# Optimization experiments

Measured on AMD Instinct MI355X. Metric: run time of the kernel, lower is better.

## Reference

```python
import jax, jax.numpy as jnp
import numpy as np

B, N, IN_DIM = 32, 8192, 128
H, C = 4, 32
NEG_SLOPE = 0.2


def _xavier(key, shape, fan_in, fan_out):
    limit = np.sqrt(6.0 / (fan_in + fan_out))
    return jax.random.uniform(key, shape, minval=-limit, maxval=limit, dtype=jnp.float32)


def setup_inputs() -> dict:
    key = jax.random.key(0)
    k_x, k_wl, k_wr, k_att = jax.random.split(key, 4)
    x = jax.random.normal(k_x, (B, N, IN_DIM), dtype=jnp.float32)
    W_l = _xavier(k_wl, (IN_DIM, H * C), IN_DIM, H * C)
    b_l = jnp.zeros((H * C,), dtype=jnp.float32)
    W_r = _xavier(k_wr, (IN_DIM, H * C), IN_DIM, H * C)
    b_r = jnp.zeros((H * C,), dtype=jnp.float32)
    att = _xavier(k_att, (H, C), H, C)
    return {"x": x, "W_l": W_l, "b_l": b_l, "W_r": W_r, "b_r": b_r, "att": att}


def reference(x, W_l, b_l, W_r, b_r, att):
    Bs, Ns, _ = x.shape
    # Dense projections -> [B, N, H, C]
    x_l = (x @ W_l + b_l).reshape(Bs, Ns, H, C)
    x_r = (x @ W_r + b_r).reshape(Bs, Ns, H, C)
    # GATv2 additive score for edges (j -> center 0): LeakyReLU(x_l[0] + x_r[j])
    e = jax.nn.leaky_relu(x_l[:, :1, :, :] + x_r, negative_slope=NEG_SLOPE)  # [B,N,H,C]
    logits = jnp.einsum('bnhc,hc->bnh', e, att)  # [B,N,H]
    alpha = jax.nn.softmax(logits, axis=1)
    # Weighted aggregation into the center node; others keep their self-loop x_r
    m_center = jnp.sum(alpha[..., None] * x_r, axis=1, keepdims=True)  # [B,1,H,C]
    out = x_r.at[:, :1, :, :].set(m_center)
    return out.reshape(Bs, Ns, H * C)
```

## Files before the change

kernel.cpp:

```cpp
#include <hip/hip_runtime.h>

#define BATCH 32
#define NROWS 8192
#define IND   128
#define HC    128
#define NEG   0.2f
#define NBLK  32
#define ROWS  64
#define ITERS (NROWS / (NBLK * ROWS))
#define PART_STRIDE 136

typedef __attribute__((ext_vector_type(8))) short short8;
typedef __attribute__((ext_vector_type(4))) float f32x4;

__device__ __forceinline__ unsigned short f2bf(float f) {
    unsigned u = __float_as_uint(f);
    u += 0x7FFFu + ((u >> 16) & 1u);
    return (unsigned short)(u >> 16);
}
__device__ __forceinline__ unsigned pack2(float a, float b) {
    return (unsigned)f2bf(a) | ((unsigned)f2bf(b) << 16);
}

__global__ void gat_center(const float* __restrict__ x, const float* __restrict__ Wl,
                           const float* __restrict__ bl, float* __restrict__ xl0)
{
    const int b = blockIdx.x, t = threadIdx.x;
    __shared__ float xrow[128];
    xrow[t] = x[(size_t)b * NROWS * IND + t];
    __syncthreads();
    float acc = bl[t];
#pragma unroll 16
    for (int k = 0; k < 128; ++k) acc = fmaf(xrow[k], Wl[k * 128 + t], acc);
    xl0[b * 128 + t] = acc;
}

__global__ __launch_bounds__(256, 2) void gat_main(
    const float* __restrict__ x, const float* __restrict__ Wr,
    const float* __restrict__ br, const float* __restrict__ att,
    const float* __restrict__ xl0, float* __restrict__ out,
    float* __restrict__ part)
{
    const int tid  = threadIdx.x;
    const int lane = tid & 63;
    const int wv   = tid >> 6;
    const int b    = blockIdx.x >> 5;
    const int blk  = blockIdx.x & (NBLK - 1);

    __shared__ unsigned short WrT[128 * 128];
    __shared__ float ubuf[64 * 132];
    __shared__ float w_s[64][4];
    __shared__ float wmax_s[4][4];
    __shared__ float wsum_s[4][4];
    __shared__ float Mrun_s[4], Srun_s[4], scale_s[4];
    __shared__ float Prun_s[128];
    __shared__ float ptmp_s[2][128];
    __shared__ float xl0_s[128], att_s[128], br_s[128];

    unsigned short* Asw = (unsigned short*)ubuf;
    float (*xr_s)[132]  = (float(*)[132])ubuf;

    for (int i = tid; i < 128 * 128; i += 256) {
        int n = i & 127, k = i >> 7;
        WrT[n * 128 + (k ^ ((n & 7) << 3))] = f2bf(Wr[k * 128 + n]);
    }
    if (tid < 128) {
        xl0_s[tid]  = xl0[b * 128 + tid];
        att_s[tid]  = att[tid];
        br_s[tid]   = br[tid];
        Prun_s[tid] = 0.f;
    }
    if (tid < 4) { Mrun_s[tid] = -INFINITY; Srun_s[tid] = 0.f; }
    __syncthreads();

    const int lr = tid >> 2, lh = tid & 3;

    for (int it = 0; it < ITERS; ++it) {
        const int n0 = blk * (ITERS * ROWS) + it * ROWS;
        const float* xrow0 = x + ((size_t)b * NROWS + n0) * IND;

#pragma unroll
        for (int ii = 0; ii < 4; ++ii) {
            int ci = tid + ii * 256;
            int r  = ci >> 4;
            int kc = (ci & 15) << 3;
            float4 f0 = *(const float4*)(xrow0 + r * IND + kc);
            float4 f1 = *(const float4*)(xrow0 + r * IND + kc + 4);
            uint4 u;
            u.x = pack2(f0.x, f0.y); u.y = pack2(f0.z, f0.w);
            u.z = pack2(f1.x, f1.y); u.w = pack2(f1.z, f1.w);
            *(uint4*)&Asw[r * 128 + (kc ^ ((r & 7) << 3))] = u;
        }
        __syncthreads();

        f32x4 acc[8];
#pragma unroll
        for (int i = 0; i < 8; ++i) acc[i] = (f32x4){0.f, 0.f, 0.f, 0.f};
        {
            const int rA   = wv * 16 + (lane & 15);
            const int ksel = lane >> 4;
            short8 afr[4];
#pragma unroll
            for (int ks = 0; ks < 4; ++ks) {
                int k0 = ks * 32 + ksel * 8;
                afr[ks] = *(const short8*)&Asw[rA * 128 + (k0 ^ ((rA & 7) << 3))];
            }
            const int nb = lane & 15;
#pragma unroll
            for (int nt = 0; nt < 8; ++nt) {
                const int n = nt * 16 + nb;
                const unsigned short* bp = &WrT[n * 128];
                const int sw = (n & 7) << 3;
#pragma unroll
                for (int ks = 0; ks < 4; ++ks) {
                    int k0 = ks * 32 + ksel * 8;
                    short8 bfr = *(const short8*)&bp[k0 ^ sw];
                    acc[nt] = __builtin_amdgcn_mfma_f32_16x16x32_bf16(afr[ks], bfr, acc[nt], 0, 0, 0);
                }
            }
        }
        __syncthreads();

        {
            const int rowb = wv * 16 + (lane >> 4) * 4;
            const int colb = lane & 15;
#pragma unroll
            for (int nt = 0; nt < 8; ++nt) {
                const int col  = nt * 16 + colb;
                const float bias = br_s[col];
#pragma unroll
                for (int rg = 0; rg < 4; ++rg)
                    xr_s[rowb + rg][col] = acc[nt][rg] + bias;
            }
        }
        __syncthreads();

        {
            float* ob = out + ((size_t)b * NROWS + n0) * HC;
#pragma unroll
            for (int j = 0; j < 8; ++j) {
                int idx = tid + j * 256;
                int row = idx >> 5, c4 = (idx & 31) << 2;
                *(float4*)(ob + row * HC + c4) = *(const float4*)&xr_s[row][c4];
            }
        }

        float lg = 0.f;
        {
            const float* xp = &xr_s[lr][lh * 32];
            const float* ap = &att_s[lh * 32];
            const float* qp = &xl0_s[lh * 32];
#pragma unroll
            for (int c4 = 0; c4 < 32; c4 += 4) {
                float4 xv = *(const float4*)(xp + c4);
                float4 av = *(const float4*)(ap + c4);
                float4 qv = *(const float4*)(qp + c4);
                float v0 = qv.x + xv.x; v0 = v0 > 0.f ? v0 : NEG * v0;
                float v1 = qv.y + xv.y; v1 = v1 > 0.f ? v1 : NEG * v1;
                float v2 = qv.z + xv.z; v2 = v2 > 0.f ? v2 : NEG * v2;
                float v3 = qv.w + xv.w; v3 = v3 > 0.f ? v3 : NEG * v3;
                lg = fmaf(v0, av.x, fmaf(v1, av.y, fmaf(v2, av.z, fmaf(v3, av.w, lg))));
            }
        }

        float mx = lg;
#pragma unroll
        for (int mk = 4; mk < 64; mk <<= 1) mx = fmaxf(mx, __shfl_xor(mx, mk));
        if (lane < 4) wmax_s[wv][lane] = mx;
        __syncthreads();

        const float Mblk = fmaxf(fmaxf(wmax_s[0][lh], wmax_s[1][lh]),
                                 fmaxf(wmax_s[2][lh], wmax_s[3][lh]));
        const float Mold = Mrun_s[lh];
        const float Mnew = fmaxf(Mold, Mblk);
        const float w    = __expf(lg - Mnew);
        w_s[lr][lh] = w;
        float swv = w;
#pragma unroll
        for (int mk = 4; mk < 64; mk <<= 1) swv += __shfl_xor(swv, mk);
        if (lane < 4) wsum_s[wv][lane] = swv;
        __syncthreads();

        if (tid < 4) {
            const float sc = __expf(Mold - Mnew);
            scale_s[tid] = sc;
            Srun_s[tid]  = Srun_s[tid] * sc +
                (wsum_s[0][tid] + wsum_s[1][tid] + wsum_s[2][tid] + wsum_s[3][tid]);
            Mrun_s[tid]  = Mnew;
        }
        {
            const int hc = tid & 127, half = tid >> 7;
            const int h2 = hc >> 5;
            float accp = 0.f;
#pragma unroll 8
            for (int i2 = 0; i2 < 32; ++i2) {
                int rr = half * 32 + i2;
                accp = fmaf(w_s[rr][h2], xr_s[rr][hc], accp);
            }
            ptmp_s[half][hc] = accp;
        }
        __syncthreads();
        if (tid < 128)
            Prun_s[tid] = Prun_s[tid] * scale_s[tid >> 5] + ptmp_s[0][tid] + ptmp_s[1][tid];
        __syncthreads();
    }

    float* pb = part + (size_t)(b * NBLK + blk) * PART_STRIDE;
    if (tid < 4)   { pb[tid] = Mrun_s[tid]; pb[4 + tid] = Srun_s[tid]; }
    if (tid < 128) pb[8 + tid] = Prun_s[tid];
}

__global__ void gat_final(const float* __restrict__ part, float* __restrict__ out)
{
    const int b = blockIdx.x, t = threadIdx.x;
    const int h = t >> 5;
    const float* pb = part + (size_t)b * NBLK * PART_STRIDE;
    float Mg = -INFINITY;
    for (int i = 0; i < NBLK; ++i) Mg = fmaxf(Mg, pb[i * PART_STRIDE + h]);
    float Sg = 0.f, Pg = 0.f;
    for (int i = 0; i < NBLK; ++i) {
        const float sc = __expf(pb[i * PART_STRIDE + h] - Mg);
        Sg += pb[i * PART_STRIDE + 4 + h] * sc;
        Pg  = fmaf(pb[i * PART_STRIDE + 8 + t], sc, Pg);
    }
    out[(size_t)b * NROWS * HC + t] = Pg / Sg;
}

extern "C" void kernel_launch(void* const* d_in, const int* in_sizes, int n_in,
                              void* d_out, int out_size, void* d_ws, size_t ws_size,
                              hipStream_t stream)
{
    const float* x   = (const float*)d_in[0];
    const float* Wl  = (const float*)d_in[1];
    const float* bl  = (const float*)d_in[2];
    const float* Wr  = (const float*)d_in[3];
    const float* br  = (const float*)d_in[4];
    const float* att = (const float*)d_in[5];
    float* out = (float*)d_out;

    float* xl0  = (float*)d_ws;
    float* part = xl0 + BATCH * 128;

    gat_center<<<BATCH, 128, 0, stream>>>(x, Wl, bl, xl0);
    gat_main<<<BATCH * NBLK, 256, 0, stream>>>(x, Wr, br, att, xl0, out, part);
    gat_final<<<BATCH, 128, 0, stream>>>(part, out);
}
```

Baseline: 74.03 us.

## Keep Wr fragments in registers and drop the shared-memory weight tile

Each wave now owns 32 output columns and loads its bf16 Wr fragments into registers once, before the row loop, instead of re-reading the transposed weight tile from LDS on every iteration. This frees the 32 KB WrT shared buffer, since the weights are staged temporarily in the reused ubuf, and raises the launch bound to 4 blocks per CU for higher occupancy. The trade-off is more VGPRs held for the B fragments, and each wave now reloads A fragments for all four row tiles. Register pressure under the tighter launch bound could cause spills.

```diff
diff --git a/kernel.cpp b/kernel.cpp
--- a/kernel.cpp
+++ b/kernel.cpp
@@ -35,7 +35,7 @@
     xl0[b * 128 + t] = acc;
 }
 
-__global__ __launch_bounds__(256, 2) void gat_main(
+__global__ __launch_bounds__(256, 4) void gat_main(
     const float* __restrict__ x, const float* __restrict__ Wr,
     const float* __restrict__ br, const float* __restrict__ att,
     const float* __restrict__ xl0, float* __restrict__ out,
@@ -47,7 +47,6 @@
     const int b    = blockIdx.x >> 5;
     const int blk  = blockIdx.x & (NBLK - 1);
 
-    __shared__ unsigned short WrT[128 * 128];
     __shared__ float ubuf[64 * 132];
     __shared__ float w_s[64][4];
     __shared__ float wmax_s[4][4];
@@ -62,7 +61,7 @@
 
     for (int i = tid; i < 128 * 128; i += 256) {
         int n = i & 127, k = i >> 7;
-        WrT[n * 128 + (k ^ ((n & 7) << 3))] = f2bf(Wr[k * 128 + n]);
+        Asw[n * 128 + (k ^ ((n & 7) << 3))] = f2bf(Wr[k * 128 + n]);
     }
     if (tid < 128) {
         xl0_s[tid]  = xl0[b * 128 + tid];
@@ -71,6 +70,22 @@
         Prun_s[tid] = 0.f;
     }
     if (tid < 4) { Mrun_s[tid] = -INFINITY; Srun_s[tid] = 0.f; }
+    __syncthreads();
+
+    short8 bfr[2][4];
+    {
+        const int ksel = lane >> 4;
+#pragma unroll
+        for (int ct = 0; ct < 2; ++ct) {
+            const int n  = wv * 32 + ct * 16 + (lane & 15);
+            const int sw = (n & 7) << 3;
+#pragma unroll
+            for (int ks = 0; ks < 4; ++ks) {
+                int k0 = ks * 32 + ksel * 8;
+                bfr[ct][ks] = *(const short8*)&Asw[n * 128 + (k0 ^ sw)];
+            }
+        }
+    }
     __syncthreads();
 
     const int lr = tid >> 2, lh = tid & 3;
@@ -93,45 +108,46 @@
         }
         __syncthreads();
 
-        f32x4 acc[8];
-#pragma unroll
-        for (int i = 0; i < 8; ++i) acc[i] = (f32x4){0.f, 0.f, 0.f, 0.f};
-        {
-            const int rA   = wv * 16 + (lane & 15);
+        f32x4 acc[4][2];
+#pragma unroll
+        for (int i = 0; i < 4; ++i)
+#pragma unroll
+            for (int j = 0; j < 2; ++j) acc[i][j] = (f32x4){0.f, 0.f, 0.f, 0.f};
+        {
             const int ksel = lane >> 4;
-            short8 afr[4];
-#pragma unroll
-            for (int ks = 0; ks < 4; ++ks) {
-                int k0 = ks * 32 + ksel * 8;
-                afr[ks] = *(const short8*)&Asw[rA * 128 + (k0 ^ ((rA & 7) << 3))];
-            }
-            const int nb = lane & 15;
-#pragma unroll
-            for (int nt = 0; nt < 8; ++nt) {
-                const int n = nt * 16 + nb;
-                const unsigned short* bp = &WrT[n * 128];
-                const int sw = (n & 7) << 3;
+#pragma unroll
+            for (int rt = 0; rt < 4; ++rt) {
+                const int rA  = rt * 16 + (lane & 15);
+                const int swa = (rA & 7) << 3;
+                short8 afr[4];
 #pragma unroll
                 for (int ks = 0; ks < 4; ++ks) {
                     int k0 = ks * 32 + ksel * 8;
-                    short8 bfr = *(const short8*)&bp[k0 ^ sw];
-                    acc[nt] = __builtin_amdgcn_mfma_f32_16x16x32_bf16(afr[ks], bfr, acc[nt], 0, 0, 0);
+                    afr[ks] = *(const short8*)&Asw[rA * 128 + (k0 ^ swa)];
                 }
-            }
-        }
-        __syncthreads();
-
-        {
-            const int rowb = wv * 16 + (lane >> 4) * 4;
-            const int colb = lane & 15;
-#pragma unroll
-            for (int nt = 0; nt < 8; ++nt) {
-                const int col  = nt * 16 + colb;
-                const float bias = br_s[col];
-#pragma unroll
-                for (int rg = 0; rg < 4; ++rg)
-                    xr_s[rowb + rg][col] = acc[nt][rg] + bias;
-            }
+#pragma unroll
+                for (int ct = 0; ct < 2; ++ct)
+#pragma unroll
+                    for (int ks = 0; ks < 4; ++ks)
+                        acc[rt][ct] = __builtin_amdgcn_mfma_f32_16x16x32_bf16(
+                            afr[ks], bfr[ct][ks], acc[rt][ct], 0, 0, 0);
+            }
+        }
+        __syncthreads();
+
+        {
+            const int rq = (lane >> 4) * 4;
+            const int cb = lane & 15;
+#pragma unroll
+            for (int rt = 0; rt < 4; ++rt)
+#pragma unroll
+                for (int ct = 0; ct < 2; ++ct) {
+                    const int col  = wv * 32 + ct * 16 + cb;
+                    const float bias = br_s[col];
+#pragma unroll
+                    for (int rg = 0; rg < 4; ++rg)
+                        xr_s[rt * 16 + rq + rg][col] = acc[rt][ct][rg] + bias;
+                }
         }
         __syncthreads();
 
```

New measurement: 75.93 us. 1.03x slower.

## Make each wave an independent online-softmax unit with register-resident weights

Applied to the files above, without the earlier changes.

Restructures gat_main so each wave processes its own 128-row slice as 8 tiles of 16 rows, keeping the bf16 W_r fragments in registers instead of LDS. Each wave loads its x fragments directly from global into registers, prefetching the next tile during compute. Softmax max/sum and the weighted aggregation are done per wave with shuffles, which removes all block-level barriers in the loop. The price is very high register pressure from 32 short8 B fragments plus accumulators and prefetch buffers. It also produces twice as many partials for the final reduction kernel.

```diff
diff --git a/kernel.cpp b/kernel.cpp
--- a/kernel.cpp
+++ b/kernel.cpp
@@ -5,13 +5,15 @@
 #define IND   128
 #define HC    128
 #define NEG   0.2f
-#define NBLK  32
-#define ROWS  64
-#define ITERS (NROWS / (NBLK * ROWS))
+#define TILES 8
+#define TROWS 16
+#define WPB   64
 #define PART_STRIDE 136
 
 typedef __attribute__((ext_vector_type(8))) short short8;
 typedef __attribute__((ext_vector_type(4))) float f32x4;
+
+#define CFENCE() asm volatile("" ::: "memory")
 
 __device__ __forceinline__ unsigned short f2bf(float f) {
     unsigned u = __float_as_uint(f);
@@ -44,110 +46,109 @@
     const int tid  = threadIdx.x;
     const int lane = tid & 63;
     const int wv   = tid >> 6;
-    const int b    = blockIdx.x >> 5;
-    const int blk  = blockIdx.x & (NBLK - 1);
-
-    __shared__ unsigned short WrT[128 * 128];
-    __shared__ float ubuf[64 * 132];
-    __shared__ float w_s[64][4];
-    __shared__ float wmax_s[4][4];
-    __shared__ float wsum_s[4][4];
-    __shared__ float Mrun_s[4], Srun_s[4], scale_s[4];
-    __shared__ float Prun_s[128];
-    __shared__ float ptmp_s[2][128];
-    __shared__ float xl0_s[128], att_s[128], br_s[128];
-
-    unsigned short* Asw = (unsigned short*)ubuf;
-    float (*xr_s)[132]  = (float(*)[132])ubuf;
-
-    for (int i = tid; i < 128 * 128; i += 256) {
-        int n = i & 127, k = i >> 7;
-        WrT[n * 128 + (k ^ ((n & 7) << 3))] = f2bf(Wr[k * 128 + n]);
-    }
-    if (tid < 128) {
-        xl0_s[tid]  = xl0[b * 128 + tid];
-        att_s[tid]  = att[tid];
-        br_s[tid]   = br[tid];
-        Prun_s[tid] = 0.f;
-    }
-    if (tid < 4) { Mrun_s[tid] = -INFINITY; Srun_s[tid] = 0.f; }
+    const int b    = blockIdx.x >> 4;
+    const int wu   = (blockIdx.x & 15) * 4 + wv;
+
+    __shared__ float lds[4 * 2176 + 256];
+    float* xr_s  = lds + wv * 2176;
+    float* w_s   = xr_s + 2112;
+    float* att_s = lds + 4 * 2176;
+    float* xl0_s = att_s + 128;
+
+    if (tid < 128) { att_s[tid] = att[tid]; xl0_s[tid] = xl0[b * 128 + tid]; }
+
+    const int l15 = lane & 15, ksel = lane >> 4;
+
+    short8 bfr[8][4];
+#pragma unroll
+    for (int nt = 0; nt < 8; ++nt) {
+        const int n = nt * 16 + l15;
+#pragma unroll
+        for (int ks = 0; ks < 4; ++ks) {
+            const float* wp = Wr + (size_t)(ks * 32 + ksel * 8) * HC + n;
+            float v0 = wp[0 * HC], v1 = wp[1 * HC], v2 = wp[2 * HC], v3 = wp[3 * HC];
+            float v4 = wp[4 * HC], v5 = wp[5 * HC], v6 = wp[6 * HC], v7 = wp[7 * HC];
+            union { short8 s; unsigned u[4]; } u;
+            u.u[0] = pack2(v0, v1); u.u[1] = pack2(v2, v3);
+            u.u[2] = pack2(v4, v5); u.u[3] = pack2(v6, v7);
+            bfr[nt][ks] = u.s;
+        }
+    }
+    float bi[8];
+#pragma unroll
+    for (int nt = 0; nt < 8; ++nt) bi[nt] = br[nt * 16 + l15];
+
     __syncthreads();
 
-    const int lr = tid >> 2, lh = tid & 3;
-
-    for (int it = 0; it < ITERS; ++it) {
-        const int n0 = blk * (ITERS * ROWS) + it * ROWS;
-        const float* xrow0 = x + ((size_t)b * NROWS + n0) * IND;
-
-#pragma unroll
-        for (int ii = 0; ii < 4; ++ii) {
-            int ci = tid + ii * 256;
-            int r  = ci >> 4;
-            int kc = (ci & 15) << 3;
-            float4 f0 = *(const float4*)(xrow0 + r * IND + kc);
-            float4 f1 = *(const float4*)(xrow0 + r * IND + kc + 4);
-            uint4 u;
-            u.x = pack2(f0.x, f0.y); u.y = pack2(f0.z, f0.w);
-            u.z = pack2(f1.x, f1.y); u.w = pack2(f1.z, f1.w);
-            *(uint4*)&Asw[r * 128 + (kc ^ ((r & 7) << 3))] = u;
-        }
-        __syncthreads();
-
+    const size_t row0 = (size_t)b * NROWS + (size_t)wu * (TILES * TROWS);
+    const int lr = lane >> 2, lh = lane & 3;
+    const int pc0 = lane, pc1 = lane + 64;
+    const int h0 = pc0 >> 5, h1 = 2 + (pc0 >> 5);
+
+    short8 afr[4];
+    {
+        const float* sp = x + (row0 + l15) * IND;
+        float4 pf0[4][2];
+#pragma unroll
+        for (int ks = 0; ks < 4; ++ks) {
+            pf0[ks][0] = *(const float4*)(sp + ks * 32 + ksel * 8);
+            pf0[ks][1] = *(const float4*)(sp + ks * 32 + ksel * 8 + 4);
+        }
+#pragma unroll
+        for (int ks = 0; ks < 4; ++ks) {
+            union { short8 s; unsigned u[4]; } u;
+            u.u[0] = pack2(pf0[ks][0].x, pf0[ks][0].y);
+            u.u[1] = pack2(pf0[ks][0].z, pf0[ks][0].w);
+            u.u[2] = pack2(pf0[ks][1].x, pf0[ks][1].y);
+            u.u[3] = pack2(pf0[ks][1].z, pf0[ks][1].w);
+            afr[ks] = u.s;
+        }
+    }
+
+    float Mrun = -INFINITY, Srun = 0.f, P0 = 0.f, P1 = 0.f;
+
+    for (int t = 0; t < TILES; ++t) {
         f32x4 acc[8];
 #pragma unroll
-        for (int i = 0; i < 8; ++i) acc[i] = (f32x4){0.f, 0.f, 0.f, 0.f};
+        for (int nt = 0; nt < 8; ++nt) acc[nt] = (f32x4){0.f, 0.f, 0.f, 0.f};
+#pragma unroll
+        for (int nt = 0; nt < 8; ++nt)
+#pragma unroll
+            for (int ks = 0; ks < 4; ++ks)
+                acc[nt] = __builtin_amdgcn_mfma_f32_16x16x32_bf16(
+                    afr[ks], bfr[nt][ks], acc[nt], 0, 0, 0);
+
+        float4 pf[4][2];
+        if (t + 1 < TILES) {
+            const float* sp = x + (row0 + (size_t)(t + 1) * TROWS + l15) * IND;
+#pragma unroll
+            for (int ks = 0; ks < 4; ++ks) {
+                pf[ks][0] = *(const float4*)(sp + ks * 32 + ksel * 8);
+                pf[ks][1] = *(const float4*)(sp + ks * 32 + ksel * 8 + 4);
+            }
+        }
+
+#pragma unroll
+        for (int nt = 0; nt < 8; ++nt)
+#pragma unroll
+            for (int rg = 0; rg < 4; ++rg)
+                xr_s[(ksel * 4 + rg) * 132 + nt * 16 + l15] = acc[nt][rg] + bi[nt];
+        CFENCE();
+
         {
-            const int rA   = wv * 16 + (lane & 15);
-            const int ksel = lane >> 4;
-            short8 afr[4];
-#pragma unroll
-            for (int ks = 0; ks < 4; ++ks) {
-                int k0 = ks * 32 + ksel * 8;
-                afr[ks] = *(const short8*)&Asw[rA * 128 + (k0 ^ ((rA & 7) << 3))];
-            }
-            const int nb = lane & 15;
-#pragma unroll
-            for (int nt = 0; nt < 8; ++nt) {
-                const int n = nt * 16 + nb;
-                const unsigned short* bp = &WrT[n * 128];
-                const int sw = (n & 7) << 3;
-#pragma unroll
-                for (int ks = 0; ks < 4; ++ks) {
-                    int k0 = ks * 32 + ksel * 8;
-                    short8 bfr = *(const short8*)&bp[k0 ^ sw];
-                    acc[nt] = __builtin_amdgcn_mfma_f32_16x16x32_bf16(afr[ks], bfr, acc[nt], 0, 0, 0);
-                }
-            }
-        }
-        __syncthreads();
-
-        {
-            const int rowb = wv * 16 + (lane >> 4) * 4;
-            const int colb = lane & 15;
-#pragma unroll
-            for (int nt = 0; nt < 8; ++nt) {
-                const int col  = nt * 16 + colb;
-                const float bias = br_s[col];
-#pragma unroll
-                for (int rg = 0; rg < 4; ++rg)
-                    xr_s[rowb + rg][col] = acc[nt][rg] + bias;
-            }
-        }
-        __syncthreads();
-
-        {
-            float* ob = out + ((size_t)b * NROWS + n0) * HC;
+            float* ob = out + (row0 + (size_t)t * TROWS) * HC;
 #pragma unroll
             for (int j = 0; j < 8; ++j) {
-                int idx = tid + j * 256;
-                int row = idx >> 5, c4 = (idx & 31) << 2;
-                *(float4*)(ob + row * HC + c4) = *(const float4*)&xr_s[row][c4];
+                const int row = 2 * j + (lane >> 5);
+                const int cc  = (lane & 31) * 4;
+                *(float4*)(ob + (size_t)row * HC + cc) =
+                    *(const float4*)&xr_s[row * 132 + cc];
             }
         }
 
         float lg = 0.f;
         {
-            const float* xp = &xr_s[lr][lh * 32];
+            const float* xp = &xr_s[lr * 132 + lh * 32];
             const float* ap = &att_s[lh * 32];
             const float* qp = &xl0_s[lh * 32];
 #pragma unroll
@@ -162,63 +163,67 @@
                 lg = fmaf(v0, av.x, fmaf(v1, av.y, fmaf(v2, av.z, fmaf(v3, av.w, lg))));
             }
         }
-
         float mx = lg;
-#pragma unroll
-        for (int mk = 4; mk < 64; mk <<= 1) mx = fmaxf(mx, __shfl_xor(mx, mk));
-        if (lane < 4) wmax_s[wv][lane] = mx;
-        __syncthreads();
-
-        const float Mblk = fmaxf(fmaxf(wmax_s[0][lh], wmax_s[1][lh]),
-                                 fmaxf(wmax_s[2][lh], wmax_s[3][lh]));
-        const float Mold = Mrun_s[lh];
-        const float Mnew = fmaxf(Mold, Mblk);
+        mx = fmaxf(mx, __shfl_xor(mx, 4));
+        mx = fmaxf(mx, __shfl_xor(mx, 8));
+        mx = fmaxf(mx, __shfl_xor(mx, 16));
+        mx = fmaxf(mx, __shfl_xor(mx, 32));
+        const float Mnew = fmaxf(Mrun, mx);
         const float w    = __expf(lg - Mnew);
-        w_s[lr][lh] = w;
-        float swv = w;
-#pragma unroll
-        for (int mk = 4; mk < 64; mk <<= 1) swv += __shfl_xor(swv, mk);
-        if (lane < 4) wsum_s[wv][lane] = swv;
-        __syncthreads();
-
-        if (tid < 4) {
-            const float sc = __expf(Mold - Mnew);
-            scale_s[tid] = sc;
-            Srun_s[tid]  = Srun_s[tid] * sc +
-                (wsum_s[0][tid] + wsum_s[1][tid] + wsum_s[2][tid] + wsum_s[3][tid]);
-            Mrun_s[tid]  = Mnew;
-        }
+        float sw = w;
+        sw += __shfl_xor(sw, 4);  sw += __shfl_xor(sw, 8);
+        sw += __shfl_xor(sw, 16); sw += __shfl_xor(sw, 32);
+        const float sc = __expf(Mrun - Mnew);
+        Srun = Srun * sc + sw;
+        Mrun = Mnew;
+        w_s[lh * 16 + lr] = w;
+        CFENCE();
+
         {
-            const int hc = tid & 127, half = tid >> 7;
-            const int h2 = hc >> 5;
-            float accp = 0.f;
-#pragma unroll 8
-            for (int i2 = 0; i2 < 32; ++i2) {
-                int rr = half * 32 + i2;
-                accp = fmaf(w_s[rr][h2], xr_s[rr][hc], accp);
-            }
-            ptmp_s[half][hc] = accp;
-        }
-        __syncthreads();
-        if (tid < 128)
-            Prun_s[tid] = Prun_s[tid] * scale_s[tid >> 5] + ptmp_s[0][tid] + ptmp_s[1][tid];
-        __syncthreads();
-    }
-
-    float* pb = part + (size_t)(b * NBLK + blk) * PART_STRIDE;
-    if (tid < 4)   { pb[tid] = Mrun_s[tid]; pb[4 + tid] = Srun_s[tid]; }
-    if (tid < 128) pb[8 + tid] = Prun_s[tid];
+            const float sc0 = __shfl(sc, h0);
+            const float sc1 = __shfl(sc, h1);
+            const float* w0 = &w_s[h0 * 16];
+            const float* w1 = &w_s[h1 * 16];
+            float a0 = 0.f, a1 = 0.f;
+#pragma unroll
+            for (int r = 0; r < 16; ++r) {
+                a0 = fmaf(w0[r], xr_s[r * 132 + pc0], a0);
+                a1 = fmaf(w1[r], xr_s[r * 132 + pc1], a1);
+            }
+            P0 = P0 * sc0 + a0;
+            P1 = P1 * sc1 + a1;
+        }
+
+        if (t + 1 < TILES) {
+#pragma unroll
+            for (int ks = 0; ks < 4; ++ks) {
+                union { short8 s; unsigned u[4]; } u;
+                u.u[0] = pack2(pf[ks][0].x, pf[ks][0].y);
+                u.u[1] = pack2(pf[ks][0].z, pf[ks][0].w);
+                u.u[2] = pack2(pf[ks][1].x, pf[ks][1].y);
+                u.u[3] = pack2(pf[ks][1].z, pf[ks][1].w);
+                afr[ks] = u.s;
+            }
+        }
+    }
+
+    float* pb = part + (size_t)(b * WPB + wu) * PART_STRIDE;
+    if (lane < 4) { pb[lane] = Mrun; pb[4 + lane] = Srun; }
+    pb[8 + pc0] = P0;
+    pb[8 + pc1] = P1;
 }
 
 __global__ void gat_final(const float* __restrict__ part, float* __restrict__ out)
 {
     const int b = blockIdx.x, t = threadIdx.x;
     const int h = t >> 5;
-    const float* pb = part + (size_t)b * NBLK * PART_STRIDE;
+    const float* pb = part + (size_t)b * WPB * PART_STRIDE;
     float Mg = -INFINITY;
-    for (int i = 0; i < NBLK; ++i) Mg = fmaxf(Mg, pb[i * PART_STRIDE + h]);
+#pragma unroll 4
+    for (int i = 0; i < WPB; ++i) Mg = fmaxf(Mg, pb[i * PART_STRIDE + h]);
     float Sg = 0.f, Pg = 0.f;
-    for (int i = 0; i < NBLK; ++i) {
+#pragma unroll 4
+    for (int i = 0; i < WPB; ++i) {
         const float sc = __expf(pb[i * PART_STRIDE + h] - Mg);
         Sg += pb[i * PART_STRIDE + 4 + h] * sc;
         Pg  = fmaf(pb[i * PART_STRIDE + 8 + t], sc, Pg);
@@ -242,6 +247,6 @@
     float* part = xl0 + BATCH * 128;
 
     gat_center<<<BATCH, 128, 0, stream>>>(x, Wl, bl, xl0);
-    gat_main<<<BATCH * NBLK, 256, 0, stream>>>(x, Wr, br, att, xl0, out, part);
+    gat_main<<<BATCH * 16, 256, 0, stream>>>(x, Wr, br, att, xl0, out, part);
     gat_final<<<BATCH, 128, 0, stream>>>(part, out);
 }
```

Measured after the change: 119.1 us. 1.61x slower.
